# Performance work log

Measured on AMD Instinct MI355X. Metric: run time of the kernel, lower is better.

Reference implementation:

```python
import jax, jax.numpy as jnp
import numpy as np

LN_EPS = 1e-5


def setup_inputs() -> dict:
    key = jax.random.key(0)
    k1, k2, k3, k4, k5 = jax.random.split(key, 5)
    N, D, E, T = 100000, 128, 400000, 4  # nodes, feat dim, edges per etype, n etypes
    feat = jax.random.normal(k1, (N, D), dtype=jnp.float32)
    W = jax.random.normal(k2, (T, D, D), dtype=jnp.float32)
    Wf = jax.random.normal(k3, (T, D, 2 * D), dtype=jnp.float32)
    ln_w = jnp.ones((D,), dtype=jnp.float32)
    ln_b = jnp.zeros((D,), dtype=jnp.float32)
    src = jax.random.randint(k4, (T, E), 0, N, dtype=jnp.int32)
    dst = jax.random.randint(k5, (T, E), 0, N, dtype=jnp.int32)
    return {"feat": feat, "W": W, "Wf": Wf, "ln_w": ln_w, "ln_b": ln_b, "src": src, "dst": dst}


def reference(feat, W, Wf, ln_w, ln_b, src, dst):
    N, D = feat.shape
    T = W.shape[0]
    h = jnp.zeros((N, D), dtype=feat.dtype)
    for t in range(T):  # small fixed loop over edge types (structurally distinct weights)
        msg = feat @ W[t]                    # [N, D] per-src-node projection
        fw = feat @ Wf[t]                    # [N, 2D] FiLM params (dst ntype == src ntype)
        gamma, beta = fw[:, :D], fw[:, D:]
        m = jax.nn.relu(gamma * msg + beta)  # node-wise FiLM + ReLU, pre-scatter
        # copy_u -> gather message at edge src; fn.sum -> segment-sum into dst
        h = h + jax.ops.segment_sum(m[src[t]], dst[t], num_segments=N)
    # LayerNorm (elementwise affine); dropout omitted (eval mode)
    mu = jnp.mean(h, axis=-1, keepdims=True)
    var = jnp.mean(jnp.square(h - mu), axis=-1, keepdims=True)
    out = (h - mu) * jax.lax.rsqrt(var + LN_EPS) * ln_w + ln_b
    return out
```

## Files before the change

kernel.cpp:

```cpp
#include <hip/hip_runtime.h>
#include <hip/hip_bf16.h>

#define DD 128
#define LN_EPS 1e-5f
#define BCAP 3072
#define MAXBIN 1024
#define CHUNK 4096
#define SPLIT 4

typedef __bf16 bf16x8 __attribute__((ext_vector_type(8)));
typedef float f32x4 __attribute__((ext_vector_type(4)));

__device__ __forceinline__ float bflo(unsigned int u) { return __uint_as_float(u << 16); }
__device__ __forceinline__ float bfhi(unsigned int u) { return __uint_as_float(u & 0xffff0000u); }

__device__ __forceinline__ void gload_lds16(const void* g, void* lds) {
    __builtin_amdgcn_global_load_lds(
        (const __attribute__((address_space(1))) unsigned int*)g,
        (__attribute__((address_space(3))) unsigned int*)lds, 16, 0, 0);
}

__global__ __launch_bounds__(256) void k_pack_feat(const float* __restrict__ f,
                                                   unsigned short* __restrict__ fb, int n8) {
    int i = blockIdx.x * 256 + threadIdx.x;
    if (i >= n8) return;
    const float4* p = (const float4*)f + (size_t)i * 2;
    float4 v0 = p[0], v1 = p[1];
    float vv[8] = {v0.x, v0.y, v0.z, v0.w, v1.x, v1.y, v1.z, v1.w};
    unsigned short u[8];
#pragma unroll
    for (int j = 0; j < 8; j++) {
        __hip_bfloat16 b = __float2bfloat16(vv[j]);
        u[j] = *reinterpret_cast<unsigned short*>(&b);
    }
    uint4 o;
    o.x = u[0] | ((unsigned)u[1] << 16);
    o.y = u[2] | ((unsigned)u[3] << 16);
    o.z = u[4] | ((unsigned)u[5] << 16);
    o.w = u[6] | ((unsigned)u[7] << 16);
    ((uint4*)fb)[i] = o;
}

__global__ __launch_bounds__(256) void k_pack_w(const float* __restrict__ W,
                                                const float* __restrict__ Wf,
                                                unsigned short* __restrict__ wcat) {
    int i = blockIdx.x * 256 + threadIdx.x;
    if (i >= 4 * 384 * 128) return;
    int t = i / (384 * 128);
    int r = i % (384 * 128);
    int c = r / 128, k = r % 128;
    float v = (c < 128) ? W[((size_t)t * 128 + k) * 128 + c]
                        : Wf[((size_t)t * 128 + k) * 256 + (c - 128)];
    __hip_bfloat16 b = __float2bfloat16(v);
    wcat[i] = *reinterpret_cast<unsigned short*>(&b);
}

__global__ __launch_bounds__(256) void k_hist2(const int* __restrict__ dst,
                                               int* __restrict__ H, int E4, int NBLK, int NBIN) {
    __shared__ int h[MAXBIN];
    const int b = blockIdx.x;
    for (int j = threadIdx.x; j < NBIN; j += 256) h[j] = 0;
    __syncthreads();
    int base = b * CHUNK;
    int end = base + CHUNK < E4 ? base + CHUNK : E4;
    for (int i = base + threadIdx.x; i < end; i += 256) atomicAdd(&h[dst[i] >> 7], 1);
    __syncthreads();
    for (int j = threadIdx.x; j < NBIN; j += 256) H[(size_t)j * NBLK + b] = h[j];
}

__global__ __launch_bounds__(256) void k_scanbin(int* __restrict__ H, int* __restrict__ C,
                                                 int NBLK, int NBIN) {
    const int wv = (blockIdx.x * 256 + threadIdx.x) >> 6;
    const int lane = threadIdx.x & 63;
    if (wv >= NBIN) return;
    int* row = H + (size_t)wv * NBLK;
    int run = 0;
    for (int base = 0; base < NBLK; base += 64) {
        int idx = base + lane;
        int v = (idx < NBLK) ? row[idx] : 0;
        int s = v;
#pragma unroll
        for (int o = 1; o < 64; o <<= 1) {
            int u = __shfl_up(s, o, 64);
            if (lane >= o) s += u;
        }
        if (idx < NBLK) row[idx] = run + s - v;
        run += __shfl(s, 63, 64);
    }
    if (lane == 0) C[wv] = run;
}

__global__ __launch_bounds__(1024) void k_scan(const int* __restrict__ cnt,
                                               int* __restrict__ off, int NB) {
    __shared__ int s[1024];
    int tid = threadIdx.x;
    s[tid] = (tid < NB) ? cnt[tid] : 0;
    __syncthreads();
    for (int st = 1; st < 1024; st <<= 1) {
        int t = s[tid];
        int a = (tid >= st) ? s[tid - st] : 0;
        __syncthreads();
        s[tid] = t + a;
        __syncthreads();
    }
    if (tid < NB) {
        off[tid] = s[tid] - cnt[tid];
        if (tid == NB - 1) off[NB] = s[tid];
    }
}

__global__ __launch_bounds__(256) void k_place2(const int* __restrict__ src,
                                                const int* __restrict__ dst,
                                                const int* __restrict__ H,
                                                const int* __restrict__ binoff,
                                                unsigned int* __restrict__ rec,
                                                int N, int E, int E4, int NBLK, int NBIN) {
    __shared__ int fill[MAXBIN];
    const int b = blockIdx.x;
    for (int j = threadIdx.x; j < NBIN; j += 256)
        fill[j] = binoff[j] + H[(size_t)j * NBLK + b];
    __syncthreads();
    int base = b * CHUNK;
    int end = base + CHUNK < E4 ? base + CHUNK : E4;
    for (int i = base + threadIdx.x; i < end; i += 256) {
        int d = dst[i];
        int t = i / E;
        unsigned int r = ((unsigned)(d & 127) << 19) | (unsigned)(t * N + src[i]);
        int pos = atomicAdd(&fill[d >> 7], 1);
        rec[pos] = r;
    }
}

__global__ __launch_bounds__(256, 2) void k_gemm_film(const unsigned short* __restrict__ featb,
                                                      const unsigned short* __restrict__ wcat,
                                                      unsigned short* __restrict__ m, int N,
                                                      int NT) {
    __shared__ unsigned char smem[2 * 16384];
    const int t = blockIdx.y;
    const int tid = threadIdx.x;
    const int w = tid >> 6, lane = tid & 63;
    const int lr = lane & 15, kg = lane >> 4;
    const int cbase = w * 32;

    const unsigned short* wt = wcat + (size_t)t * 384 * 128;
    bf16x8 B[4][3][2];
#pragma unroll
    for (int kkI = 0; kkI < 4; kkI++)
#pragma unroll
        for (int mat = 0; mat < 3; mat++)
#pragma unroll
            for (int cj = 0; cj < 2; cj++) {
                int col = mat * 128 + cbase + cj * 16 + lr;
                B[kkI][mat][cj] = *(const bf16x8*)(wt + (size_t)col * 128 + kkI * 32 + kg * 8);
            }

    auto stage = [&](int buf, int r0) {
#pragma unroll
        for (int it = 0; it < 4; it++) {
            int row = it * 16 + w * 4 + (lane >> 4);
            int gr = r0 + row;
            if (gr >= N) gr = N - 1;
            int x = ((lane & 15) * 16) ^ ((row & 7) << 4);
            const unsigned char* g = (const unsigned char*)featb + (size_t)gr * 256 + x;
            gload_lds16(g, smem + buf * 16384 + it * 4096 + w * 1024);
        }
    };

    unsigned short* mt = m + (size_t)t * N * DD;
    int buf = 0;
    int tile = blockIdx.x;
    if (tile < NT) stage(0, tile * 64);

    for (; tile < NT; tile += gridDim.x) {
        __syncthreads();
        int nxt = tile + gridDim.x;
        if (nxt < NT) stage(buf ^ 1, nxt * 64);

        const unsigned char* sm = smem + buf * 16384;
        f32x4 acc[4][3][2] = {};
#pragma unroll
        for (int kkI = 0; kkI < 4; kkI++) {
            bf16x8 a[4];
#pragma unroll
            for (int mi = 0; mi < 4; mi++) {
                int row = mi * 16 + lr;
                int kb = kkI * 64 + kg * 16;
                a[mi] = *(const bf16x8*)(sm + row * 256 + (kb ^ ((row & 7) << 4)));
            }
#pragma unroll
            for (int mi = 0; mi < 4; mi++)
#pragma unroll
                for (int mat = 0; mat < 3; mat++)
#pragma unroll
                    for (int cj = 0; cj < 2; cj++)
                        acc[mi][mat][cj] = __builtin_amdgcn_mfma_f32_16x16x32_bf16(
                            a[mi], B[kkI][mat][cj], acc[mi][mat][cj], 0, 0, 0);
        }

        const int r0 = tile * 64;
#pragma unroll
        for (int mi = 0; mi < 4; mi++)
#pragma unroll
            for (int cj = 0; cj < 2; cj++)
#pragma unroll
                for (int r = 0; r < 4; r++) {
                    int row = r0 + mi * 16 + kg * 4 + r;
                    if (row < N) {
                        float v = acc[mi][1][cj][r] * acc[mi][0][cj][r] + acc[mi][2][cj][r];
                        v = fmaxf(v, 0.0f);
                        __hip_bfloat16 b = __float2bfloat16(v);
                        mt[(size_t)row * DD + cbase + cj * 16 + lr] =
                            *reinterpret_cast<unsigned short*>(&b);
                    }
                }
        buf ^= 1;
    }
}

__global__ __launch_bounds__(256) void k_sort_agg_ln(const unsigned int* __restrict__ rec,
                                                     const int* __restrict__ binoff,
                                                     const unsigned int* __restrict__ m32,
                                                     const float* __restrict__ lnw,
                                                     const float* __restrict__ lnb,
                                                     float* __restrict__ out, int N) {
    __shared__ int lcnt[128], soff[128], sfill[128], tmp[128];
    __shared__ unsigned int sorted[BCAP];
    const int b = blockIdx.x / SPLIT, sub = blockIdx.x % SPLIT;
    const int tid = threadIdx.x;
    const int s0 = binoff[b];
    int n = binoff[b + 1] - s0;
    if (n > BCAP) n = BCAP;

    if (tid < 128) lcnt[tid] = 0;
    __syncthreads();
    for (int j = tid; j < n; j += 256) atomicAdd(&lcnt[rec[s0 + j] >> 19], 1);
    __syncthreads();
    if (tid < 128) tmp[tid] = lcnt[tid];
    __syncthreads();
    for (int st = 1; st < 128; st <<= 1) {
        int t = 0, a = 0;
        if (tid < 128) {
            t = tmp[tid];
            a = (tid >= st) ? tmp[tid - st] : 0;
        }
        __syncthreads();
        if (tid < 128) tmp[tid] = t + a;
        __syncthreads();
    }
    if (tid < 128) {
        int ex = tmp[tid] - lcnt[tid];
        soff[tid] = ex;
        sfill[tid] = ex;
    }
    __syncthreads();
    for (int j = tid; j < n; j += 256) {
        unsigned int r = rec[s0 + j];
        int p = atomicAdd(&sfill[r >> 19], 1);
        sorted[p] = r & 0x7FFFFu;
    }
    __syncthreads();

    const int wv = tid >> 6, lane = tid & 63;
#pragma unroll 1
    for (int i = 0; i < 128 / SPLIT / 4; i++) {
        int d7 = sub * (128 / SPLIT) + i * 4 + wv;
        int node = b * 128 + d7;
        if (node >= N) continue;
        int e0 = soff[d7], en = lcnt[d7];
        float a0 = 0.f, a1 = 0.f;
        int e = 0;
        for (; e + 4 <= en; e += 4) {
            unsigned g0 = sorted[e0 + e], g1 = sorted[e0 + e + 1];
            unsigned g2 = sorted[e0 + e + 2], g3 = sorted[e0 + e + 3];
            unsigned p0 = m32[(size_t)g0 * 64 + lane];
            unsigned p1 = m32[(size_t)g1 * 64 + lane];
            unsigned p2 = m32[(size_t)g2 * 64 + lane];
            unsigned p3 = m32[(size_t)g3 * 64 + lane];
            a0 += bflo(p0) + bflo(p1) + bflo(p2) + bflo(p3);
            a1 += bfhi(p0) + bfhi(p1) + bfhi(p2) + bfhi(p3);
        }
        for (; e < en; e++) {
            unsigned p0 = m32[(size_t)sorted[e0 + e] * 64 + lane];
            a0 += bflo(p0);
            a1 += bfhi(p0);
        }
        float sum = a0 + a1, ssq = a0 * a0 + a1 * a1;
#pragma unroll
        for (int o = 1; o < 64; o <<= 1) {
            sum += __shfl_xor(sum, o, 64);
            ssq += __shfl_xor(ssq, o, 64);
        }
        float mu = sum * (1.0f / 128.0f);
        float var = ssq * (1.0f / 128.0f) - mu * mu;
        float rstd = rsqrtf(var + LN_EPS);
        int d0 = lane * 2;
        float o0 = (a0 - mu) * rstd * lnw[d0] + lnb[d0];
        float o1 = (a1 - mu) * rstd * lnw[d0 + 1] + lnb[d0 + 1];
        *(float2*)(out + (size_t)node * DD + d0) = make_float2(o0, o1);
    }
}

extern "C" void kernel_launch(void* const* d_in, const int* in_sizes, int n_in,
                              void* d_out, int out_size, void* d_ws, size_t ws_size,
                              hipStream_t stream) {
    const float* feat = (const float*)d_in[0];
    const float* W    = (const float*)d_in[1];
    const float* Wf   = (const float*)d_in[2];
    const float* lnw  = (const float*)d_in[3];
    const float* lnb  = (const float*)d_in[4];
    const int* src    = (const int*)d_in[5];
    const int* dst    = (const int*)d_in[6];
    float* out = (float*)d_out;

    const int N = in_sizes[0] / DD;
    const int E = in_sizes[5] / 4;
    const int E4 = 4 * E;
    const int NB = (N + 127) >> 7;
    const int NBLK = (E4 + CHUNK - 1) / CHUNK;
    const int NT = (N + 63) / 64;

    size_t off = 0;
    char* ws = (char*)d_ws;
    auto alloc = [&](size_t bytes) -> void* {
        void* p = ws + off;
        off += (bytes + 255) & ~(size_t)255;
        return p;
    };
    unsigned short* m     = (unsigned short*)alloc((size_t)4 * N * DD * 2);
    unsigned short* featb = (unsigned short*)alloc((size_t)N * DD * 2);
    unsigned short* wcat  = (unsigned short*)alloc((size_t)4 * 384 * 128 * 2);
    int* H      = (int*)alloc((size_t)NB * NBLK * 4);
    int* C      = (int*)alloc((size_t)NB * 4);
    int* binoff = (int*)alloc((size_t)(NB + 1) * 4);
    unsigned int* rec = (unsigned int*)alloc((size_t)E4 * 4);
    if (off > ws_size) return;

    int n8 = N * DD / 8;
    k_pack_feat<<<(n8 + 255) / 256, 256, 0, stream>>>(feat, featb, n8);
    k_pack_w<<<(4 * 384 * 128 + 255) / 256, 256, 0, stream>>>(W, Wf, wcat);
    k_hist2<<<NBLK, 256, 0, stream>>>(dst, H, E4, NBLK, NB);
    k_scanbin<<<(NB * 64 + 255) / 256, 256, 0, stream>>>(H, C, NBLK, NB);
    k_scan<<<1, 1024, 0, stream>>>(C, binoff, NB);
    k_place2<<<NBLK, 256, 0, stream>>>(src, dst, H, binoff, rec, N, E, E4, NBLK, NB);
    dim3 gg(128, 4);
    k_gemm_film<<<gg, 256, 0, stream>>>(featb, wcat, m, N, NT);
    k_sort_agg_ln<<<NB * SPLIT, 256, 0, stream>>>(rec, binoff, (const unsigned int*)m, lnw, lnb, out, N);
}
```

Measured before the change: 183.0 us.

## Split per-bin sort into separate kernel and aggregate per node with 8-byte gathers

```diff
diff --git a/kernel.cpp b/kernel.cpp
--- a/kernel.cpp
+++ b/kernel.cpp
@@ -6,7 +6,6 @@
 #define BCAP 3072
 #define MAXBIN 1024
 #define CHUNK 4096
-#define SPLIT 4
 
 typedef __bf16 bf16x8 __attribute__((ext_vector_type(8)));
 typedef float f32x4 __attribute__((ext_vector_type(4)));
@@ -131,6 +130,56 @@
     }
 }
 
+__global__ __launch_bounds__(256) void k_sortout(const unsigned int* __restrict__ rec,
+                                                 const int* __restrict__ binoff,
+                                                 unsigned int* __restrict__ sortedg,
+                                                 int* __restrict__ nodestart,
+                                                 int* __restrict__ nodedeg, int N) {
+    __shared__ int lcnt[128], soff[128], sfill[128], tmp[128];
+    __shared__ unsigned int sorted[BCAP];
+    const int b = blockIdx.x, tid = threadIdx.x;
+    const int s0 = binoff[b];
+    int n = binoff[b + 1] - s0;
+    if (n > BCAP) n = BCAP;
+
+    if (tid < 128) lcnt[tid] = 0;
+    __syncthreads();
+    for (int j = tid; j < n; j += 256) atomicAdd(&lcnt[rec[s0 + j] >> 19], 1);
+    __syncthreads();
+    if (tid < 128) tmp[tid] = lcnt[tid];
+    __syncthreads();
+    for (int st = 1; st < 128; st <<= 1) {
+        int t = 0, a = 0;
+        if (tid < 128) {
+            t = tmp[tid];
+            a = (tid >= st) ? tmp[tid - st] : 0;
+        }
+        __syncthreads();
+        if (tid < 128) tmp[tid] = t + a;
+        __syncthreads();
+    }
+    if (tid < 128) {
+        int ex = tmp[tid] - lcnt[tid];
+        soff[tid] = ex;
+        sfill[tid] = ex;
+    }
+    __syncthreads();
+    for (int j = tid; j < n; j += 256) {
+        unsigned int r = rec[s0 + j];
+        int p = atomicAdd(&sfill[r >> 19], 1);
+        sorted[p] = r & 0x7FFFFu;
+    }
+    __syncthreads();
+    for (int j = tid; j < n; j += 256) sortedg[s0 + j] = sorted[j];
+    if (tid < 128) {
+        int node = b * 128 + tid;
+        if (node < N) {
+            nodestart[node] = s0 + soff[tid];
+            nodedeg[node] = lcnt[tid];
+        }
+    }
+}
+
 __global__ __launch_bounds__(256, 2) void k_gemm_film(const unsigned short* __restrict__ featb,
                                                       const unsigned short* __restrict__ wcat,
                                                       unsigned short* __restrict__ m, int N,
@@ -217,86 +266,68 @@
     }
 }
 
-__global__ __launch_bounds__(256) void k_sort_agg_ln(const unsigned int* __restrict__ rec,
-                                                     const int* __restrict__ binoff,
-                                                     const unsigned int* __restrict__ m32,
-                                                     const float* __restrict__ lnw,
-                                                     const float* __restrict__ lnb,
-                                                     float* __restrict__ out, int N) {
-    __shared__ int lcnt[128], soff[128], sfill[128], tmp[128];
-    __shared__ unsigned int sorted[BCAP];
-    const int b = blockIdx.x / SPLIT, sub = blockIdx.x % SPLIT;
-    const int tid = threadIdx.x;
-    const int s0 = binoff[b];
-    int n = binoff[b + 1] - s0;
-    if (n > BCAP) n = BCAP;
-
-    if (tid < 128) lcnt[tid] = 0;
-    __syncthreads();
-    for (int j = tid; j < n; j += 256) atomicAdd(&lcnt[rec[s0 + j] >> 19], 1);
-    __syncthreads();
-    if (tid < 128) tmp[tid] = lcnt[tid];
-    __syncthreads();
-    for (int st = 1; st < 128; st <<= 1) {
-        int t = 0, a = 0;
-        if (tid < 128) {
-            t = tmp[tid];
-            a = (tid >= st) ? tmp[tid - st] : 0;
-        }
-        __syncthreads();
-        if (tid < 128) tmp[tid] = t + a;
-        __syncthreads();
-    }
-    if (tid < 128) {
-        int ex = tmp[tid] - lcnt[tid];
-        soff[tid] = ex;
-        sfill[tid] = ex;
-    }
-    __syncthreads();
-    for (int j = tid; j < n; j += 256) {
-        unsigned int r = rec[s0 + j];
-        int p = atomicAdd(&sfill[r >> 19], 1);
-        sorted[p] = r & 0x7FFFFu;
-    }
-    __syncthreads();
-
-    const int wv = tid >> 6, lane = tid & 63;
-#pragma unroll 1
-    for (int i = 0; i < 128 / SPLIT / 4; i++) {
-        int d7 = sub * (128 / SPLIT) + i * 4 + wv;
-        int node = b * 128 + d7;
-        if (node >= N) continue;
-        int e0 = soff[d7], en = lcnt[d7];
-        float a0 = 0.f, a1 = 0.f;
-        int e = 0;
-        for (; e + 4 <= en; e += 4) {
-            unsigned g0 = sorted[e0 + e], g1 = sorted[e0 + e + 1];
-            unsigned g2 = sorted[e0 + e + 2], g3 = sorted[e0 + e + 3];
-            unsigned p0 = m32[(size_t)g0 * 64 + lane];
-            unsigned p1 = m32[(size_t)g1 * 64 + lane];
-            unsigned p2 = m32[(size_t)g2 * 64 + lane];
-            unsigned p3 = m32[(size_t)g3 * 64 + lane];
-            a0 += bflo(p0) + bflo(p1) + bflo(p2) + bflo(p3);
-            a1 += bfhi(p0) + bfhi(p1) + bfhi(p2) + bfhi(p3);
-        }
-        for (; e < en; e++) {
-            unsigned p0 = m32[(size_t)sorted[e0 + e] * 64 + lane];
-            a0 += bflo(p0);
-            a1 += bfhi(p0);
-        }
-        float sum = a0 + a1, ssq = a0 * a0 + a1 * a1;
-#pragma unroll
-        for (int o = 1; o < 64; o <<= 1) {
-            sum += __shfl_xor(sum, o, 64);
-            ssq += __shfl_xor(ssq, o, 64);
-        }
-        float mu = sum * (1.0f / 128.0f);
-        float var = ssq * (1.0f / 128.0f) - mu * mu;
-        float rstd = rsqrtf(var + LN_EPS);
-        int d0 = lane * 2;
-        float o0 = (a0 - mu) * rstd * lnw[d0] + lnb[d0];
-        float o1 = (a1 - mu) * rstd * lnw[d0 + 1] + lnb[d0 + 1];
-        *(float2*)(out + (size_t)node * DD + d0) = make_float2(o0, o1);
+__global__ __launch_bounds__(256) void k_agg_ln(const unsigned int* __restrict__ sortedg,
+                                                const int* __restrict__ nodestart,
+                                                const int* __restrict__ nodedeg,
+                                                const uint2* __restrict__ m2,
+                                                const float* __restrict__ lnw,
+                                                const float* __restrict__ lnb,
+                                                float* __restrict__ out, int N) {
+    const int wv = threadIdx.x >> 6, lane = threadIdx.x & 63;
+    const int node = blockIdx.x * 4 + wv;
+    if (node >= N) return;
+    const int start = nodestart[node], deg = nodedeg[node];
+    const int half = lane >> 5, sl = lane & 31;
+
+    float a0 = 0.f, a1 = 0.f, a2 = 0.f, a3 = 0.f;
+    int e = 0;
+    for (; e + 8 <= deg; e += 8) {
+        unsigned g0 = sortedg[start + e + 0 + half];
+        unsigned g1 = sortedg[start + e + 2 + half];
+        unsigned g2 = sortedg[start + e + 4 + half];
+        unsigned g3 = sortedg[start + e + 6 + half];
+        uint2 p0 = m2[(size_t)g0 * 32 + sl];
+        uint2 p1 = m2[(size_t)g1 * 32 + sl];
+        uint2 p2 = m2[(size_t)g2 * 32 + sl];
+        uint2 p3 = m2[(size_t)g3 * 32 + sl];
+        a0 += bflo(p0.x) + bflo(p1.x) + bflo(p2.x) + bflo(p3.x);
+        a1 += bfhi(p0.x) + bfhi(p1.x) + bfhi(p2.x) + bfhi(p3.x);
+        a2 += bflo(p0.y) + bflo(p1.y) + bflo(p2.y) + bflo(p3.y);
+        a3 += bfhi(p0.y) + bfhi(p1.y) + bfhi(p2.y) + bfhi(p3.y);
+    }
+    for (; e < deg; e += 2) {
+        int idx = e + half;
+        if (idx < deg) {
+            uint2 p = m2[(size_t)sortedg[start + idx] * 32 + sl];
+            a0 += bflo(p.x);
+            a1 += bfhi(p.x);
+            a2 += bflo(p.y);
+            a3 += bfhi(p.y);
+        }
+    }
+    a0 += __shfl_xor(a0, 32, 64);
+    a1 += __shfl_xor(a1, 32, 64);
+    a2 += __shfl_xor(a2, 32, 64);
+    a3 += __shfl_xor(a3, 32, 64);
+    float s = a0 + a1 + a2 + a3;
+    float ss = a0 * a0 + a1 * a1 + a2 * a2 + a3 * a3;
+#pragma unroll
+    for (int o = 1; o < 32; o <<= 1) {
+        s += __shfl_xor(s, o, 64);
+        ss += __shfl_xor(ss, o, 64);
+    }
+    float mu = s * (1.0f / 128.0f);
+    float var = ss * (1.0f / 128.0f) - mu * mu;
+    float rstd = rsqrtf(var + LN_EPS);
+    if (half == 0) {
+        float4 w4 = ((const float4*)lnw)[sl];
+        float4 b4 = ((const float4*)lnb)[sl];
+        float4 o4;
+        o4.x = (a0 - mu) * rstd * w4.x + b4.x;
+        o4.y = (a1 - mu) * rstd * w4.y + b4.y;
+        o4.z = (a2 - mu) * rstd * w4.z + b4.z;
+        o4.w = (a3 - mu) * rstd * w4.w + b4.w;
+        ((float4*)(out + (size_t)node * DD))[sl] = o4;
     }
 }
 
@@ -332,7 +363,10 @@
     int* H      = (int*)alloc((size_t)NB * NBLK * 4);
     int* C      = (int*)alloc((size_t)NB * 4);
     int* binoff = (int*)alloc((size_t)(NB + 1) * 4);
-    unsigned int* rec = (unsigned int*)alloc((size_t)E4 * 4);
+    unsigned int* rec     = (unsigned int*)alloc((size_t)E4 * 4);
+    unsigned int* sortedg = (unsigned int*)alloc((size_t)E4 * 4);
+    int* nodestart = (int*)alloc((size_t)N * 4);
+    int* nodedeg   = (int*)alloc((size_t)N * 4);
     if (off > ws_size) return;
 
     int n8 = N * DD / 8;
@@ -342,7 +376,9 @@
     k_scanbin<<<(NB * 64 + 255) / 256, 256, 0, stream>>>(H, C, NBLK, NB);
     k_scan<<<1, 1024, 0, stream>>>(C, binoff, NB);
     k_place2<<<NBLK, 256, 0, stream>>>(src, dst, H, binoff, rec, N, E, E4, NBLK, NB);
+    k_sortout<<<NB, 256, 0, stream>>>(rec, binoff, sortedg, nodestart, nodedeg, N);
     dim3 gg(128, 4);
     k_gemm_film<<<gg, 256, 0, stream>>>(featb, wcat, m, N, NT);
-    k_sort_agg_ln<<<NB * SPLIT, 256, 0, stream>>>(rec, binoff, (const unsigned int*)m, lnw, lnb, out, N);
-}
+    k_agg_ln<<<(N + 3) / 4, 256, 0, stream>>>(sortedg, nodestart, nodedeg,
+                                              (const uint2*)m, lnw, lnb, out, N);
+}
```

Result: faster. 176.5 us (-3.6%).
